# Performance work log

Measured on AMD Instinct MI355X. Metric: run time of the kernel, lower is better.

Reference implementation:

```python
import jax, jax.numpy as jnp
import numpy as np

NUM_HEADS = 12
SIZE_PER_HEAD = 64
NEG_INF = -10000.0


def setup_inputs() -> dict:
    key = jax.random.key(0)
    k1, k2, k3, k4 = jax.random.split(key, 4)
    B, S, D = 2, 2048, 768
    x = jax.random.normal(k1, (B, S, D), dtype=jnp.float32)
    mask = jax.random.randint(k2, (B, S, S), 0, 2, dtype=jnp.int32)
    std = 0.02
    Wq = jax.random.normal(k3, (D, NUM_HEADS * SIZE_PER_HEAD), dtype=jnp.float32) * std
    Wk = jax.random.normal(k4, (D, NUM_HEADS * SIZE_PER_HEAD), dtype=jnp.float32) * std
    bq = jnp.zeros((NUM_HEADS * SIZE_PER_HEAD,), dtype=jnp.float32)
    bk = jnp.zeros((NUM_HEADS * SIZE_PER_HEAD,), dtype=jnp.float32)
    return {"x": x, "mask": mask, "Wq": Wq, "bq": bq, "Wk": Wk, "bk": bk}


def reference(x, mask, Wq, bq, Wk, bk):
    B, S, D = x.shape
    H, dh = NUM_HEADS, SIZE_PER_HEAD
    # Dense query/key projections (no activation), then split heads: [B,H,S,dh]
    q = (x @ Wq + bq).reshape(B, S, H, dh).transpose(0, 2, 1, 3)
    k = (x @ Wk + bk).reshape(B, S, H, dh).transpose(0, 2, 1, 3)
    # Scaled dot-product scores: [B,H,S,S]
    scores = jnp.einsum("bhqd,bhkd->bhqk", q, k) / jnp.sqrt(jnp.float32(dh))
    # Mask: [B,S,S] -> [B,1,S,S]; zeros get large negative additive bias
    adder = (1.0 - mask.astype(jnp.float32))[:, None, :, :] * NEG_INF
    probs = jax.nn.softmax(scores + adder, axis=-1)
    # dropout is identity at inference (training=None)
    return probs
```

## Files before the change

### kernel.cpp

```cpp
#include <hip/hip_runtime.h>
#include <stdint.h>

#define NUM_HEADS 12
#define DH 64
#define SEQ 2048
#define BATCH 2
#define DM 768
#define NQK 1536
#define LOG2E 1.44269504088896340736f

typedef short short8 __attribute__((ext_vector_type(8)));
typedef short short4_t __attribute__((ext_vector_type(4)));
typedef float f32x4 __attribute__((ext_vector_type(4)));

__device__ __forceinline__ short bf16_rne(float f) {
    union { float f; uint32_t u; } v; v.f = f;
    return (short)((v.u + 0x7FFFu + ((v.u >> 16) & 1u)) >> 16);
}

__global__ __launch_bounds__(256) void wt_kernel(const float* __restrict__ Wq,
                                                 const float* __restrict__ Wk,
                                                 short* __restrict__ Wt) {
    __shared__ float tile[32][33];
    int n0 = blockIdx.x * 32;
    int k0 = blockIdx.y * 32;
    int tx = threadIdx.x & 31;
    int ty = threadIdx.x >> 5;
    const float* src = (n0 < DM) ? Wq : Wk;
    int nn0 = (n0 < DM) ? n0 : n0 - DM;
#pragma unroll
    for (int j = 0; j < 4; ++j) {
        int k = ty + 8 * j;
        tile[k][tx] = src[(size_t)(k0 + k) * DM + nn0 + tx];
    }
    __syncthreads();
#pragma unroll
    for (int j = 0; j < 4; ++j) {
        int n = ty + 8 * j;
        Wt[(size_t)(n0 + n) * DM + k0 + tx] = bf16_rne(tile[tx][n]);
    }
}

__global__ __launch_bounds__(256) void xb_kernel(const float* __restrict__ x,
                                                 short* __restrict__ Xb) {
    int i = (blockIdx.x * 256 + threadIdx.x) * 4;
    f32x4 v = *(const f32x4*)(x + i);
    short4_t s;
#pragma unroll
    for (int j = 0; j < 4; ++j) s[j] = bf16_rne(v[j]);
    *(short4_t*)(Xb + i) = s;
}

__global__ __launch_bounds__(256) void mpack_kernel(const int* __restrict__ mask,
                                                    unsigned long long* __restrict__ Mb) {
    int wid = (blockIdx.x * 256 + threadIdx.x) >> 6;
    int lane = threadIdx.x & 63;
    size_t base = (size_t)wid * 8;
#pragma unroll
    for (int i = 0; i < 8; ++i) {
        size_t w = base + i;
        int v = mask[w * 64 + lane];
        unsigned long long bal = __ballot(v != 0);
        if (lane == 0) Mb[w] = bal;
    }
}

__global__ __launch_bounds__(256) void proj_kernel(const short* __restrict__ Xb,
                                                   const short* __restrict__ Wt,
                                                   const float* __restrict__ bq,
                                                   const float* __restrict__ bk,
                                                   short* __restrict__ QK) {
    __shared__ short As[128 * 40];
    __shared__ short Bs[128 * 40];
    const int m0 = blockIdx.x * 128;
    const int n0 = blockIdx.y * 128;
    const int t = threadIdx.x;
    const int lane = t & 63;
    const int w = t >> 6;
    const int wr = w >> 1, wc = w & 1;
    const int lr = lane & 15;
    const int lk = lane >> 4;

    f32x4 acc[4][4] = {};

    for (int k0 = 0; k0 < DM; k0 += 32) {
#pragma unroll
        for (int j = 0; j < 2; ++j) {
            int idx = t + 256 * j;
            int row = idx >> 2;
            int ch = idx & 3;
            *(short8*)&As[row * 40 + ch * 8] =
                *(const short8*)&Xb[(size_t)(m0 + row) * DM + k0 + ch * 8];
            *(short8*)&Bs[row * 40 + ch * 8] =
                *(const short8*)&Wt[(size_t)(n0 + row) * DM + k0 + ch * 8];
        }
        __syncthreads();
        short8 a[4], bfr[4];
#pragma unroll
        for (int m = 0; m < 4; ++m)
            a[m] = *(short8*)&As[(wr * 64 + m * 16 + lr) * 40 + lk * 8];
#pragma unroll
        for (int n = 0; n < 4; ++n)
            bfr[n] = *(short8*)&Bs[(wc * 64 + n * 16 + lr) * 40 + lk * 8];
#pragma unroll
        for (int m = 0; m < 4; ++m)
#pragma unroll
            for (int n = 0; n < 4; ++n)
                acc[m][n] = __builtin_amdgcn_mfma_f32_16x16x32_bf16(a[m], bfr[n], acc[m][n], 0, 0, 0);
        __syncthreads();
    }

    const int orow = m0 + wr * 64;
    const int ocol = n0 + wc * 64;
#pragma unroll
    for (int m = 0; m < 4; ++m) {
#pragma unroll
        for (int n = 0; n < 4; ++n) {
            int col = ocol + n * 16 + lr;
            float bias = (col < DM) ? bq[col] : bk[col - DM];
            float scale = (col < DM) ? 0.125f * LOG2E : 1.0f;
#pragma unroll
            for (int r = 0; r < 4; ++r) {
                int row = orow + m * 16 + lk * 4 + r;
                QK[(size_t)row * NQK + col] = bf16_rne((acc[m][n][r] + bias) * scale);
            }
        }
    }
}

__global__ __launch_bounds__(256) void attn_kernel(const short* __restrict__ QK,
                                                   const unsigned long long* __restrict__ Mb,
                                                   float* __restrict__ out) {
    __shared__ short Ks[64 * 72];
    const int qblk = blockIdx.x;
    const int h = blockIdx.y;
    const int b = blockIdx.z;
    const int t = threadIdx.x;
    const int lane = t & 63;
    const int w = t >> 6;
    const int lr = lane & 15;
    const int lk = lane >> 4;
    const int wq = qblk * 64 + w * 16;

    short8 aq[2];
#pragma unroll
    for (int ks = 0; ks < 2; ++ks)
        aq[ks] = *(const short8*)&QK[(size_t)(b * SEQ + wq + lr) * NQK + h * DH + ks * 32 + lk * 8];

    float lrow[4] = {0.f, 0.f, 0.f, 0.f};
    const size_t mrow0 = (size_t)b * SEQ * (SEQ / 64);

    for (int kt = 0; kt < SEQ; kt += 64) {
#pragma unroll
        for (int j = 0; j < 2; ++j) {
            int idx = t + 256 * j;
            int row = idx >> 3;
            int ch = idx & 7;
            *(short8*)&Ks[row * 72 + ch * 8] =
                *(const short8*)&QK[(size_t)(b * SEQ + kt + row) * NQK + DM + h * DH + ch * 8];
        }
        __syncthreads();
        f32x4 sc[4];
#pragma unroll
        for (int nf = 0; nf < 4; ++nf) {
            short8 k0 = *(short8*)&Ks[(nf * 16 + lr) * 72 + lk * 8];
            short8 k1 = *(short8*)&Ks[(nf * 16 + lr) * 72 + 32 + lk * 8];
            f32x4 a = {0.f, 0.f, 0.f, 0.f};
            a = __builtin_amdgcn_mfma_f32_16x16x32_bf16(aq[0], k0, a, 0, 0, 0);
            a = __builtin_amdgcn_mfma_f32_16x16x32_bf16(aq[1], k1, a, 0, 0, 0);
            sc[nf] = a;
        }
#pragma unroll
        for (int r = 0; r < 4; ++r) {
            int q = wq + lk * 4 + r;
            unsigned long long mbs = Mb[mrow0 + (size_t)q * 32 + (kt >> 6)] >> lr;
            float s = 0.f;
#pragma unroll
            for (int nf = 0; nf < 4; ++nf) {
                float e = __builtin_amdgcn_exp2f(sc[nf][r]);
                s += ((mbs >> (nf * 16)) & 1ull) ? e : 0.f;
            }
            lrow[r] += s;
        }
        __syncthreads();
    }

    float inv[4];
#pragma unroll
    for (int r = 0; r < 4; ++r) {
        float l = lrow[r];
        l += __shfl_xor(l, 1, 64);
        l += __shfl_xor(l, 2, 64);
        l += __shfl_xor(l, 4, 64);
        l += __shfl_xor(l, 8, 64);
        inv[r] = 1.0f / l;
    }

    for (int kt = 0; kt < SEQ; kt += 64) {
#pragma unroll
        for (int j = 0; j < 2; ++j) {
            int idx = t + 256 * j;
            int row = idx >> 3;
            int ch = idx & 7;
            *(short8*)&Ks[row * 72 + ch * 8] =
                *(const short8*)&QK[(size_t)(b * SEQ + kt + row) * NQK + DM + h * DH + ch * 8];
        }
        __syncthreads();
        f32x4 sc[4];
#pragma unroll
        for (int nf = 0; nf < 4; ++nf) {
            short8 k0 = *(short8*)&Ks[(nf * 16 + lr) * 72 + lk * 8];
            short8 k1 = *(short8*)&Ks[(nf * 16 + lr) * 72 + 32 + lk * 8];
            f32x4 a = {0.f, 0.f, 0.f, 0.f};
            a = __builtin_amdgcn_mfma_f32_16x16x32_bf16(aq[0], k0, a, 0, 0, 0);
            a = __builtin_amdgcn_mfma_f32_16x16x32_bf16(aq[1], k1, a, 0, 0, 0);
            sc[nf] = a;
        }
#pragma unroll
        for (int r = 0; r < 4; ++r) {
            int q = wq + lk * 4 + r;
            unsigned long long mbs = Mb[mrow0 + (size_t)q * 32 + (kt >> 6)] >> lr;
            float* op = &out[((size_t)((b * NUM_HEADS + h) * SEQ + q)) * SEQ + kt + lr];
#pragma unroll
            for (int nf = 0; nf < 4; ++nf) {
                float p = __builtin_amdgcn_exp2f(sc[nf][r]) * inv[r];
                op[nf * 16] = ((mbs >> (nf * 16)) & 1ull) ? p : 0.f;
            }
        }
        __syncthreads();
    }
}

extern "C" void kernel_launch(void* const* d_in, const int* in_sizes, int n_in,
                              void* d_out, int out_size, void* d_ws, size_t ws_size,
                              hipStream_t stream) {
    (void)in_sizes; (void)n_in; (void)out_size; (void)ws_size;
    const float* x = (const float*)d_in[0];
    const int* mask = (const int*)d_in[1];
    const float* Wq = (const float*)d_in[2];
    const float* bq = (const float*)d_in[3];
    const float* Wk = (const float*)d_in[4];
    const float* bk = (const float*)d_in[5];
    float* out = (float*)d_out;

    short* Wt = (short*)d_ws;
    short* Xb = Wt + (size_t)NQK * DM;
    short* QK = Xb + (size_t)BATCH * SEQ * DM;
    unsigned long long* Mb =
        (unsigned long long*)(QK + (size_t)BATCH * SEQ * NQK);

    wt_kernel<<<dim3(NQK / 32, DM / 32), 256, 0, stream>>>(Wq, Wk, Wt);
    xb_kernel<<<dim3((BATCH * SEQ * DM) / (256 * 4)), 256, 0, stream>>>(x, Xb);
    mpack_kernel<<<dim3((BATCH * SEQ * SEQ / 64) / 32), 256, 0, stream>>>(mask, Mb);
    proj_kernel<<<dim3(BATCH * SEQ / 128, NQK / 128), 256, 0, stream>>>(Xb, Wt, bq, bk, QK);
    attn_kernel<<<dim3(SEQ / 64, NUM_HEADS, BATCH), 256, 0, stream>>>(QK, Mb, out);
}
```

Before: 173.0 us.

## Merge prep kernels into one launch, widen GEMM K-tile, stage two K tiles in attention

The weight transpose, x conversion and mask bit-packing kernels are merged into one launch that picks its branch by block index, removing two launch gaps. The projection GEMM now loads a 64-wide K slice per iteration, which halves the number of barriers and global-load rounds. The attention kernel stages 128 keys per barrier pair using two shared buffers, halving its synchronisation count. These add shared memory use and make the code more complex, which may reduce occupancy.

```diff
diff --git a/kernel.cpp b/kernel.cpp
--- a/kernel.cpp
+++ b/kernel.cpp
@@ -18,50 +18,56 @@
     return (short)((v.u + 0x7FFFu + ((v.u >> 16) & 1u)) >> 16);
 }
 
-__global__ __launch_bounds__(256) void wt_kernel(const float* __restrict__ Wq,
-                                                 const float* __restrict__ Wk,
-                                                 short* __restrict__ Wt) {
+__global__ __launch_bounds__(256) void prep_kernel(const float* __restrict__ Wq,
+                                                   const float* __restrict__ Wk,
+                                                   const float* __restrict__ x,
+                                                   const int* __restrict__ mask,
+                                                   short* __restrict__ Wt,
+                                                   short* __restrict__ Xb,
+                                                   unsigned long long* __restrict__ Mb) {
     __shared__ float tile[32][33];
-    int n0 = blockIdx.x * 32;
-    int k0 = blockIdx.y * 32;
-    int tx = threadIdx.x & 31;
-    int ty = threadIdx.x >> 5;
-    const float* src = (n0 < DM) ? Wq : Wk;
-    int nn0 = (n0 < DM) ? n0 : n0 - DM;
-#pragma unroll
-    for (int j = 0; j < 4; ++j) {
-        int k = ty + 8 * j;
-        tile[k][tx] = src[(size_t)(k0 + k) * DM + nn0 + tx];
-    }
-    __syncthreads();
-#pragma unroll
-    for (int j = 0; j < 4; ++j) {
-        int n = ty + 8 * j;
-        Wt[(size_t)(n0 + n) * DM + k0 + tx] = bf16_rne(tile[tx][n]);
-    }
-}
-
-__global__ __launch_bounds__(256) void xb_kernel(const float* __restrict__ x,
-                                                 short* __restrict__ Xb) {
-    int i = (blockIdx.x * 256 + threadIdx.x) * 4;
-    f32x4 v = *(const f32x4*)(x + i);
-    short4_t s;
-#pragma unroll
-    for (int j = 0; j < 4; ++j) s[j] = bf16_rne(v[j]);
-    *(short4_t*)(Xb + i) = s;
-}
-
-__global__ __launch_bounds__(256) void mpack_kernel(const int* __restrict__ mask,
-                                                    unsigned long long* __restrict__ Mb) {
-    int wid = (blockIdx.x * 256 + threadIdx.x) >> 6;
-    int lane = threadIdx.x & 63;
-    size_t base = (size_t)wid * 8;
-#pragma unroll
-    for (int i = 0; i < 8; ++i) {
-        size_t w = base + i;
-        int v = mask[w * 64 + lane];
-        unsigned long long bal = __ballot(v != 0);
-        if (lane == 0) Mb[w] = bal;
+    const int bid = blockIdx.x;
+    const int t = threadIdx.x;
+    if (bid < 1152) {
+        int n0 = (bid % 48) * 32;
+        int k0 = (bid / 48) * 32;
+        int tx = t & 31;
+        int ty = t >> 5;
+        const float* src = (n0 < DM) ? Wq : Wk;
+        int nn0 = (n0 < DM) ? n0 : n0 - DM;
+#pragma unroll
+        for (int j = 0; j < 4; ++j) {
+            int k = ty + 8 * j;
+            tile[k][tx] = src[(size_t)(k0 + k) * DM + nn0 + tx];
+        }
+        __syncthreads();
+#pragma unroll
+        for (int j = 0; j < 4; ++j) {
+            int n = ty + 8 * j;
+            Wt[(size_t)(n0 + n) * DM + k0 + tx] = bf16_rne(tile[tx][n]);
+        }
+    } else if (bid < 1920) {
+        size_t base = (size_t)(bid - 1152) * 4096;
+#pragma unroll
+        for (int j = 0; j < 4; ++j) {
+            size_t i = base + (size_t)(t + j * 256) * 4;
+            f32x4 v = *(const f32x4*)(x + i);
+            short4_t s;
+#pragma unroll
+            for (int e = 0; e < 4; ++e) s[e] = bf16_rne(v[e]);
+            *(short4_t*)(Xb + i) = s;
+        }
+    } else {
+        int wid = (bid - 1920) * 4 + (t >> 6);
+        int lane = t & 63;
+        size_t base = (size_t)wid * 8;
+#pragma unroll
+        for (int i = 0; i < 8; ++i) {
+            size_t w = base + i;
+            int v = mask[w * 64 + lane];
+            unsigned long long bal = __ballot(v != 0);
+            if (lane == 0) Mb[w] = bal;
+        }
     }
 }
 
@@ -70,8 +76,8 @@
                                                    const float* __restrict__ bq,
                                                    const float* __restrict__ bk,
                                                    short* __restrict__ QK) {
-    __shared__ short As[128 * 40];
-    __shared__ short Bs[128 * 40];
+    __shared__ short As[128 * 72];
+    __shared__ short Bs[128 * 72];
     const int m0 = blockIdx.x * 128;
     const int n0 = blockIdx.y * 128;
     const int t = threadIdx.x;
@@ -83,30 +89,33 @@
 
     f32x4 acc[4][4] = {};
 
-    for (int k0 = 0; k0 < DM; k0 += 32) {
-#pragma unroll
-        for (int j = 0; j < 2; ++j) {
+    for (int k0 = 0; k0 < DM; k0 += 64) {
+#pragma unroll
+        for (int j = 0; j < 4; ++j) {
             int idx = t + 256 * j;
-            int row = idx >> 2;
-            int ch = idx & 3;
-            *(short8*)&As[row * 40 + ch * 8] =
+            int row = idx >> 3;
+            int ch = idx & 7;
+            *(short8*)&As[row * 72 + ch * 8] =
                 *(const short8*)&Xb[(size_t)(m0 + row) * DM + k0 + ch * 8];
-            *(short8*)&Bs[row * 40 + ch * 8] =
+            *(short8*)&Bs[row * 72 + ch * 8] =
                 *(const short8*)&Wt[(size_t)(n0 + row) * DM + k0 + ch * 8];
         }
         __syncthreads();
-        short8 a[4], bfr[4];
-#pragma unroll
-        for (int m = 0; m < 4; ++m)
-            a[m] = *(short8*)&As[(wr * 64 + m * 16 + lr) * 40 + lk * 8];
-#pragma unroll
-        for (int n = 0; n < 4; ++n)
-            bfr[n] = *(short8*)&Bs[(wc * 64 + n * 16 + lr) * 40 + lk * 8];
-#pragma unroll
-        for (int m = 0; m < 4; ++m)
+#pragma unroll
+        for (int kk = 0; kk < 2; ++kk) {
+            short8 a[4], bfr[4];
+#pragma unroll
+            for (int m = 0; m < 4; ++m)
+                a[m] = *(short8*)&As[(wr * 64 + m * 16 + lr) * 72 + kk * 32 + lk * 8];
 #pragma unroll
             for (int n = 0; n < 4; ++n)
-                acc[m][n] = __builtin_amdgcn_mfma_f32_16x16x32_bf16(a[m], bfr[n], acc[m][n], 0, 0, 0);
+                bfr[n] = *(short8*)&Bs[(wc * 64 + n * 16 + lr) * 72 + kk * 32 + lk * 8];
+#pragma unroll
+            for (int m = 0; m < 4; ++m)
+#pragma unroll
+                for (int n = 0; n < 4; ++n)
+                    acc[m][n] = __builtin_amdgcn_mfma_f32_16x16x32_bf16(a[m], bfr[n], acc[m][n], 0, 0, 0);
+        }
         __syncthreads();
     }
 
@@ -131,7 +140,7 @@
 __global__ __launch_bounds__(256) void attn_kernel(const short* __restrict__ QK,
                                                    const unsigned long long* __restrict__ Mb,
                                                    float* __restrict__ out) {
-    __shared__ short Ks[64 * 72];
+    __shared__ short Ks[2][64 * 72];
     const int qblk = blockIdx.x;
     const int h = blockIdx.y;
     const int b = blockIdx.z;
@@ -149,38 +158,47 @@
 
     float lrow[4] = {0.f, 0.f, 0.f, 0.f};
     const size_t mrow0 = (size_t)b * SEQ * (SEQ / 64);
-
-    for (int kt = 0; kt < SEQ; kt += 64) {
-#pragma unroll
-        for (int j = 0; j < 2; ++j) {
-            int idx = t + 256 * j;
-            int row = idx >> 3;
-            int ch = idx & 7;
-            *(short8*)&Ks[row * 72 + ch * 8] =
-                *(const short8*)&QK[(size_t)(b * SEQ + kt + row) * NQK + DM + h * DH + ch * 8];
-        }
-        __syncthreads();
-        f32x4 sc[4];
-#pragma unroll
-        for (int nf = 0; nf < 4; ++nf) {
-            short8 k0 = *(short8*)&Ks[(nf * 16 + lr) * 72 + lk * 8];
-            short8 k1 = *(short8*)&Ks[(nf * 16 + lr) * 72 + 32 + lk * 8];
-            f32x4 a = {0.f, 0.f, 0.f, 0.f};
-            a = __builtin_amdgcn_mfma_f32_16x16x32_bf16(aq[0], k0, a, 0, 0, 0);
-            a = __builtin_amdgcn_mfma_f32_16x16x32_bf16(aq[1], k1, a, 0, 0, 0);
-            sc[nf] = a;
-        }
-#pragma unroll
-        for (int r = 0; r < 4; ++r) {
-            int q = wq + lk * 4 + r;
-            unsigned long long mbs = Mb[mrow0 + (size_t)q * 32 + (kt >> 6)] >> lr;
-            float s = 0.f;
+    const int srow = t >> 3, sch = t & 7;
+
+#define ATT_STAGE(KT)                                                                             \
+    {                                                                                             \
+        _Pragma("unroll") for (int tb = 0; tb < 2; ++tb) {                                        \
+            *(short8*)&Ks[tb][srow * 72 + sch * 8] =                                              \
+                *(const short8*)&QK[(size_t)(b * SEQ + (KT) + tb * 64 + srow) * NQK + DM +        \
+                                    h * DH + sch * 8];                                            \
+            *(short8*)&Ks[tb][(srow + 32) * 72 + sch * 8] =                                       \
+                *(const short8*)&QK[(size_t)(b * SEQ + (KT) + tb * 64 + srow + 32) * NQK + DM +   \
+                                    h * DH + sch * 8];                                            \
+        }                                                                                         \
+    }
+
+    for (int kt = 0; kt < SEQ; kt += 128) {
+        ATT_STAGE(kt)
+        __syncthreads();
+#pragma unroll
+        for (int tb = 0; tb < 2; ++tb) {
+            f32x4 sc[4];
 #pragma unroll
             for (int nf = 0; nf < 4; ++nf) {
-                float e = __builtin_amdgcn_exp2f(sc[nf][r]);
-                s += ((mbs >> (nf * 16)) & 1ull) ? e : 0.f;
-            }
-            lrow[r] += s;
+                short8 k0 = *(short8*)&Ks[tb][(nf * 16 + lr) * 72 + lk * 8];
+                short8 k1 = *(short8*)&Ks[tb][(nf * 16 + lr) * 72 + 32 + lk * 8];
+                f32x4 a = {0.f, 0.f, 0.f, 0.f};
+                a = __builtin_amdgcn_mfma_f32_16x16x32_bf16(aq[0], k0, a, 0, 0, 0);
+                a = __builtin_amdgcn_mfma_f32_16x16x32_bf16(aq[1], k1, a, 0, 0, 0);
+                sc[nf] = a;
+            }
+#pragma unroll
+            for (int r = 0; r < 4; ++r) {
+                int q = wq + lk * 4 + r;
+                unsigned long long mbs = Mb[mrow0 + (size_t)q * 32 + ((kt >> 6) + tb)] >> lr;
+                float s = 0.f;
+#pragma unroll
+                for (int nf = 0; nf < 4; ++nf) {
+                    float e = __builtin_amdgcn_exp2f(sc[nf][r]);
+                    s += ((mbs >> (nf * 16)) & 1ull) ? e : 0.f;
+                }
+                lrow[r] += s;
+            }
         }
         __syncthreads();
     }
@@ -196,39 +214,36 @@
         inv[r] = 1.0f / l;
     }
 
-    for (int kt = 0; kt < SEQ; kt += 64) {
-#pragma unroll
-        for (int j = 0; j < 2; ++j) {
-            int idx = t + 256 * j;
-            int row = idx >> 3;
-            int ch = idx & 7;
-            *(short8*)&Ks[row * 72 + ch * 8] =
-                *(const short8*)&QK[(size_t)(b * SEQ + kt + row) * NQK + DM + h * DH + ch * 8];
-        }
-        __syncthreads();
-        f32x4 sc[4];
-#pragma unroll
-        for (int nf = 0; nf < 4; ++nf) {
-            short8 k0 = *(short8*)&Ks[(nf * 16 + lr) * 72 + lk * 8];
-            short8 k1 = *(short8*)&Ks[(nf * 16 + lr) * 72 + 32 + lk * 8];
-            f32x4 a = {0.f, 0.f, 0.f, 0.f};
-            a = __builtin_amdgcn_mfma_f32_16x16x32_bf16(aq[0], k0, a, 0, 0, 0);
-            a = __builtin_amdgcn_mfma_f32_16x16x32_bf16(aq[1], k1, a, 0, 0, 0);
-            sc[nf] = a;
-        }
-#pragma unroll
-        for (int r = 0; r < 4; ++r) {
-            int q = wq + lk * 4 + r;
-            unsigned long long mbs = Mb[mrow0 + (size_t)q * 32 + (kt >> 6)] >> lr;
-            float* op = &out[((size_t)((b * NUM_HEADS + h) * SEQ + q)) * SEQ + kt + lr];
+    for (int kt = 0; kt < SEQ; kt += 128) {
+        ATT_STAGE(kt)
+        __syncthreads();
+#pragma unroll
+        for (int tb = 0; tb < 2; ++tb) {
+            f32x4 sc[4];
 #pragma unroll
             for (int nf = 0; nf < 4; ++nf) {
-                float p = __builtin_amdgcn_exp2f(sc[nf][r]) * inv[r];
-                op[nf * 16] = ((mbs >> (nf * 16)) & 1ull) ? p : 0.f;
-            }
-        }
-        __syncthreads();
-    }
+                short8 k0 = *(short8*)&Ks[tb][(nf * 16 + lr) * 72 + lk * 8];
+                short8 k1 = *(short8*)&Ks[tb][(nf * 16 + lr) * 72 + 32 + lk * 8];
+                f32x4 a = {0.f, 0.f, 0.f, 0.f};
+                a = __builtin_amdgcn_mfma_f32_16x16x32_bf16(aq[0], k0, a, 0, 0, 0);
+                a = __builtin_amdgcn_mfma_f32_16x16x32_bf16(aq[1], k1, a, 0, 0, 0);
+                sc[nf] = a;
+            }
+#pragma unroll
+            for (int r = 0; r < 4; ++r) {
+                int q = wq + lk * 4 + r;
+                unsigned long long mbs = Mb[mrow0 + (size_t)q * 32 + ((kt >> 6) + tb)] >> lr;
+                float* op = &out[((size_t)((b * NUM_HEADS + h) * SEQ + q)) * SEQ + kt + tb * 64 + lr];
+#pragma unroll
+                for (int nf = 0; nf < 4; ++nf) {
+                    float p = __builtin_amdgcn_exp2f(sc[nf][r]) * inv[r];
+                    op[nf * 16] = ((mbs >> (nf * 16)) & 1ull) ? p : 0.f;
+                }
+            }
+        }
+        __syncthreads();
+    }
+#undef ATT_STAGE
 }
 
 extern "C" void kernel_launch(void* const* d_in, const int* in_sizes, int n_in,
@@ -249,9 +264,7 @@
     unsigned long long* Mb =
         (unsigned long long*)(QK + (size_t)BATCH * SEQ * NQK);
 
-    wt_kernel<<<dim3(NQK / 32, DM / 32), 256, 0, stream>>>(Wq, Wk, Wt);
-    xb_kernel<<<dim3((BATCH * SEQ * DM) / (256 * 4)), 256, 0, stream>>>(x, Xb);
-    mpack_kernel<<<dim3((BATCH * SEQ * SEQ / 64) / 32), 256, 0, stream>>>(mask, Mb);
+    prep_kernel<<<dim3(6016), 256, 0, stream>>>(Wq, Wk, x, mask, Wt, Xb, Mb);
     proj_kernel<<<dim3(BATCH * SEQ / 128, NQK / 128), 256, 0, stream>>>(Xb, Wt, bq, bk, QK);
     attn_kernel<<<dim3(SEQ / 64, NUM_HEADS, BATCH), 256, 0, stream>>>(QK, Mb, out);
 }
```

Result: no change. 171.7 us (-0.8%).
